# Optimization experiments

Hardware: AMD Instinct MI355X
Metric: run time of the kernel (lower is better)

The kernel has to match this reference:

```python
import jax, jax.numpy as jnp
import numpy as np

B, S, D_IN, D_OUT = 4, 2048, 2048, 2048
EPS = 1e-10


def setup_inputs() -> dict:
    key = jax.random.key(0)
    kx, kw, kb = jax.random.split(key, 3)
    x = jax.random.normal(kx, (B, S, D_IN), dtype=jnp.float32)
    weight = jax.random.normal(kw, (D_OUT, D_IN), dtype=jnp.float32) * 0.02
    bias = jax.random.normal(kb, (D_OUT,), dtype=jnp.float32) * 0.02
    return {"x": x, "weight": weight, "bias": bias}


def reference(x, weight, bias):
    # abs-mean scale over the whole weight matrix (scalar)
    scale = jnp.mean(jnp.abs(weight))
    # ternary quantization: round(w/scale) clamped to {-1, 0, 1}
    w_t = jnp.clip(jnp.round(weight / (scale + EPS)), -1.0, 1.0)
    # straight-through estimator: forward uses w_t*scale, grad flows to weight
    w_ste = weight + jax.lax.stop_gradient(w_t * scale - weight)
    # F.linear: x @ w_ste.T + bias
    return jnp.einsum('bsi,oi->bso', x, w_ste) + bias
```

## Files before the change

kernel.cpp:

```cpp
#include <hip/hip_runtime.h>
#include <hip/hip_bf16.h>
#include <stdint.h>

#define M_DIM 8192
#define N_DIM 2048
#define K_DIM 2048
#define NT    (K_DIM / 64)

typedef float f32x4 __attribute__((ext_vector_type(4)));
typedef short bf16x8 __attribute__((ext_vector_type(8)));

typedef const __attribute__((address_space(1))) char* gp_t;
typedef __attribute__((address_space(3))) char* lp_t;

static __device__ __forceinline__ void gload_lds16(const void* g, void* l) {
  __builtin_amdgcn_global_load_lds((gp_t)(uintptr_t)g, (lp_t)(uint32_t)(uintptr_t)l, 16, 0, 0);
}

static __device__ __forceinline__ unsigned short f2bf(float f) {
  unsigned int u = __float_as_uint(f);
  unsigned int r = (u + 0x7FFFu + ((u >> 16) & 1u)) >> 16;
  return (unsigned short)r;
}

__global__ void cvt_x_absum(const float* __restrict__ x, unsigned short* __restrict__ xb,
                            const float* __restrict__ w, float* __restrict__ partials) {
  const int b = blockIdx.x;
  if (b < 16384) {
    int tid = b * 256 + threadIdx.x;
    float4 v = ((const float4*)x)[tid];
    ushort4 o;
    o.x = f2bf(v.x); o.y = f2bf(v.y); o.z = f2bf(v.z); o.w = f2bf(v.w);
    ((ushort4*)xb)[tid] = o;
  } else {
    int tid = (b - 16384) * 256 + threadIdx.x;
    const float4* w4 = (const float4*)w;
    float s = 0.f;
#pragma unroll
    for (int i = 0; i < 4; ++i) {
      float4 v = w4[tid + i * 262144];
      s += fabsf(v.x) + fabsf(v.y) + fabsf(v.z) + fabsf(v.w);
    }
#pragma unroll
    for (int off = 32; off > 0; off >>= 1) s += __shfl_down(s, off, 64);
    __shared__ float ls[4];
    if ((threadIdx.x & 63) == 0) ls[threadIdx.x >> 6] = s;
    __syncthreads();
    if (threadIdx.x == 0) partials[b - 16384] = (ls[0] + ls[1]) + (ls[2] + ls[3]);
  }
}

__global__ void quant_w(const float* __restrict__ w, const float* __restrict__ partials,
                        unsigned short* __restrict__ wt, float* __restrict__ scale_out) {
  __shared__ float ls[4];
  float s = 0.f;
#pragma unroll
  for (int i = 0; i < 4; ++i) s += partials[threadIdx.x + i * 256];
#pragma unroll
  for (int off = 32; off > 0; off >>= 1) s += __shfl_down(s, off, 64);
  if ((threadIdx.x & 63) == 0) ls[threadIdx.x >> 6] = s;
  __syncthreads();
  const float scale = ((ls[0] + ls[1]) + (ls[2] + ls[3])) * (1.0f / 4194304.0f);
  if (blockIdx.x == 0 && threadIdx.x == 0) scale_out[0] = scale;

  const float inv = 1.0f / (scale + 1e-10f);
  int tid = blockIdx.x * 256 + threadIdx.x;
  float4 v = ((const float4*)w)[tid];
  ushort4 o;
  float t;
  t = fminf(1.f, fmaxf(-1.f, rintf(v.x * inv))); o.x = f2bf(t);
  t = fminf(1.f, fmaxf(-1.f, rintf(v.y * inv))); o.y = f2bf(t);
  t = fminf(1.f, fmaxf(-1.f, rintf(v.z * inv))); o.z = f2bf(t);
  t = fminf(1.f, fmaxf(-1.f, rintf(v.w * inv))); o.w = f2bf(t);
  ((ushort4*)wt)[tid] = o;
}


#define VMCNT(n) asm volatile("s_waitcnt vmcnt(" #n ")" ::: "memory")
#define FENCE    asm volatile("" ::: "memory")
#define BARRIER  do { FENCE; __builtin_amdgcn_s_barrier(); FENCE; } while (0)

#define READ_A(base, mh, dst)                                                                   \
  do {                                                                                          \
    _Pragma("unroll") for (int i = 0; i < 4; ++i) {                                             \
      dst[i][0] = *(const bf16x8*)((base) + (wr * 128 + (mh) * 64 + i * 16) * 128 + rd0);       \
      dst[i][1] = *(const bf16x8*)((base) + (wr * 128 + (mh) * 64 + i * 16) * 128 + rd1);       \
    }                                                                                           \
  } while (0)

#define READ_B(base, nh, dst)                                                                   \
  do {                                                                                          \
    _Pragma("unroll") for (int j = 0; j < 2; ++j) {                                             \
      dst[j][0] = *(const bf16x8*)((base) + (wc * 64 + (nh) * 32 + j * 16) * 128 + rd0);        \
      dst[j][1] = *(const bf16x8*)((base) + (wc * 64 + (nh) * 32 + j * 16) * 128 + rd1);        \
    }                                                                                           \
  } while (0)

#define MFMA_Q(mh, nh, ar, br)                                                                  \
  do {                                                                                          \
    __builtin_amdgcn_s_setprio(1);                                                              \
    _Pragma("unroll") for (int i = 0; i < 4; ++i)                                               \
      _Pragma("unroll") for (int j = 0; j < 2; ++j)                                             \
        acc[(mh) * 4 + i][(nh) * 2 + j] = __builtin_amdgcn_mfma_f32_16x16x32_bf16(              \
            ar[i][0], br[j][0], acc[(mh) * 4 + i][(nh) * 2 + j], 0, 0, 0);                      \
    _Pragma("unroll") for (int i = 0; i < 4; ++i)                                               \
      _Pragma("unroll") for (int j = 0; j < 2; ++j)                                             \
        acc[(mh) * 4 + i][(nh) * 2 + j] = __builtin_amdgcn_mfma_f32_16x16x32_bf16(              \
            ar[i][1], br[j][1], acc[(mh) * 4 + i][(nh) * 2 + j], 0, 0, 0);                      \
    __builtin_amdgcn_s_setprio(0);                                                              \
  } while (0)

#define SA(bufsel, r) gload_lds16(Ag + offA[r] + ktA, ldsb + (bufsel) * 65536 + tid * 16 + (r) * 8192)
#define SB(bufsel, r) gload_lds16(Bg + offB[r] + ktB, ldsb + (bufsel) * 65536 + 32768 + tid * 16 + (r) * 8192)

#define TILE_BODY(CURSEL, NXTSEL, t)                                                            \
  do {                                                                                          \
    const char* curA = ldsb + (CURSEL) * 65536;                                                 \
    const char* curB = curA + 32768;                                                            \
    READ_A(curA, 0, a0);                                                                        \
    READ_B(curB, 0, b0);                                                                        \
    if ((t) < NT - 1) { SA(NXTSEL, 0); SA(NXTSEL, 1); }                                         \
    MFMA_Q(0, 0, a0, b0);                                                                       \
    READ_B(curB, 1, b1);                                                                        \
    if ((t) < NT - 1) { SA(NXTSEL, 2); SA(NXTSEL, 3); ktA += 128; }                             \
    MFMA_Q(0, 1, a0, b1);                                                                       \
    BARRIER;        \
    READ_A(curA, 1, a1);                                                                        \
    if ((t) < NT - 2) { SB(CURSEL, 0); SB(CURSEL, 1); }                                         \
    MFMA_Q(1, 0, a1, b0);                                                                       \
    if ((t) < NT - 2) {                                                                         \
      SB(CURSEL, 2); SB(CURSEL, 3); ktB += 128;                                                 \
      VMCNT(4);                \
    } else {                                                                                    \
      VMCNT(0);                                                                                 \
    }                                                                                           \
    MFMA_Q(1, 1, a1, b1);                                                                       \
    BARRIER;                                  \
  } while (0)

__global__ void __launch_bounds__(512, 2)
gemm_bt(const unsigned short* __restrict__ A, const unsigned short* __restrict__ Bt,
        const float* __restrict__ bias, const float* __restrict__ scale_p,
        float* __restrict__ out) {
  __shared__ __align__(16) char lds_raw[131072];
  char* ldsb = (char*)lds_raw;

  const int tid = threadIdx.x;
  const int lane = tid & 63;
  const int wid = tid >> 6;
  const int wr = wid >> 2;
  const int wc = wid & 3;
  const int l15 = lane & 15, lhi = lane >> 4;

  const int swzl = (l15 & 7) << 4;
  const int rd0 = l15 * 128 + ((lhi * 16) ^ swzl);
  const int rd1 = l15 * 128 + (((lhi * 16) ^ 64) ^ swzl);

  const int bid = blockIdx.x;
  const int swz = (bid & 7) * 32 + (bid >> 3);
  const int bm = swz >> 3;
  const int bn = swz & 7;
  const int m0 = bm << 8, n0 = bn << 8;

  const int srow = tid >> 3;
  const int scol = (((tid & 7) ^ ((tid >> 3) & 7)) << 4);
  const char* Ag = (const char*)A;
  const char* Bg = (const char*)Bt;
  uint32_t offA[4], offB[4];
#pragma unroll
  for (int r = 0; r < 4; ++r) {
    offA[r] = (uint32_t)(m0 + srow + r * 64) * (K_DIM * 2) + scol;
    offB[r] = (uint32_t)(n0 + srow + r * 64) * (K_DIM * 2) + scol;
  }
  uint32_t ktA = 0, ktB = 0;

  f32x4 acc[8][4];
#pragma unroll
  for (int m = 0; m < 8; ++m)
#pragma unroll
    for (int n = 0; n < 4; ++n) {
      f32x4 z = {0.f, 0.f, 0.f, 0.f};
      acc[m][n] = z;
    }

  SA(0, 0); SA(0, 1); SA(0, 2); SA(0, 3);
  SB(0, 0); SB(0, 1); SB(0, 2); SB(0, 3);
  ktB = 128;
  SB(1, 0); SB(1, 1); SB(1, 2); SB(1, 3);
  ktA = 128; ktB = 256;
  VMCNT(4);
  BARRIER;

  bf16x8 a0[4][2], a1[4][2], b0[2][2], b1[2][2];

  for (int it = 0; it < NT / 2; ++it) {
    const int t0 = 2 * it;
    TILE_BODY(0, 1, t0);
    TILE_BODY(1, 0, t0 + 1);
  }

  const float scale = scale_p[0];
#pragma unroll
  for (int n = 0; n < 4; ++n) {
    const int col = n0 + wc * 64 + n * 16 + l15;
    const float bv = bias[col];
#pragma unroll
    for (int m = 0; m < 8; ++m) {
      const int r0 = m0 + wr * 128 + m * 16 + lhi * 4;
      float* op = out + (size_t)r0 * N_DIM + col;
#pragma unroll
      for (int j = 0; j < 4; ++j) op[(size_t)j * N_DIM] = acc[m][n][j] * scale + bv;
    }
  }
}

extern "C" void kernel_launch(void* const* d_in, const int* in_sizes, int n_in,
                              void* d_out, int out_size, void* d_ws, size_t ws_size,
                              hipStream_t stream) {
  (void)in_sizes; (void)n_in; (void)out_size; (void)ws_size;
  const float* x    = (const float*)d_in[0];
  const float* w    = (const float*)d_in[1];
  const float* bias = (const float*)d_in[2];
  float* out = (float*)d_out;

  float* partials = (float*)d_ws;
  float* scale_slot = partials + 1024;
  unsigned short* wt = (unsigned short*)((char*)d_ws + 8192);
  unsigned short* xb = (unsigned short*)((char*)d_ws + 8192 + (size_t)N_DIM * K_DIM * 2);

  cvt_x_absum<<<17408, 256, 0, stream>>>(x, xb, w, partials);
  quant_w<<<4096, 256, 0, stream>>>(w, partials, wt, scale_slot);
  gemm_bt<<<256, 512, 0, stream>>>(xb, wt, bias, scale_slot, out);
}
```

Baseline: 82.94 us.

## Switch GEMM inner loop from 16x16x32 to 32x32x16 bf16 MFMA tiles

Replaces the 16x16x32 MFMA instructions with 32x32x16 MFMA, restructuring LDS fragment reads, accumulator layout (f32x16 per 32x32 tile) and the epilogue store mapping. Larger MFMA tiles need fewer LDS fragment reads per FLOP and fewer instruction issues, which raises compute density. The swizzled LDS read pattern changes to 32-row lanes, so bank conflicts and the epilogue's strided stores may behave differently.

```diff
diff --git a/kernel.cpp b/kernel.cpp
--- a/kernel.cpp
+++ b/kernel.cpp
@@ -8,6 +8,7 @@
 #define NT    (K_DIM / 64)
 
 typedef float f32x4 __attribute__((ext_vector_type(4)));
+typedef float f32x16 __attribute__((ext_vector_type(16)));
 typedef short bf16x8 __attribute__((ext_vector_type(8)));
 
 typedef const __attribute__((address_space(1))) char* gp_t;
@@ -82,31 +83,28 @@
 
 #define READ_A(base, mh, dst)                                                                   \
   do {                                                                                          \
-    _Pragma("unroll") for (int i = 0; i < 4; ++i) {                                             \
-      dst[i][0] = *(const bf16x8*)((base) + (wr * 128 + (mh) * 64 + i * 16) * 128 + rd0);       \
-      dst[i][1] = *(const bf16x8*)((base) + (wr * 128 + (mh) * 64 + i * 16) * 128 + rd1);       \
-    }                                                                                           \
+    _Pragma("unroll") for (int mb2 = 0; mb2 < 2; ++mb2)                                         \
+      _Pragma("unroll") for (int ks = 0; ks < 4; ++ks)                                          \
+        dst[mb2][ks] = *(const bf16x8*)((base) +                                                \
+            (wr * 128 + ((mh) * 2 + mb2) * 32 + l31) * 128 +                                    \
+            ((ks * 32 + lh1 * 16) ^ swzB));                                                     \
   } while (0)
 
 #define READ_B(base, nh, dst)                                                                   \
   do {                                                                                          \
-    _Pragma("unroll") for (int j = 0; j < 2; ++j) {                                             \
-      dst[j][0] = *(const bf16x8*)((base) + (wc * 64 + (nh) * 32 + j * 16) * 128 + rd0);        \
-      dst[j][1] = *(const bf16x8*)((base) + (wc * 64 + (nh) * 32 + j * 16) * 128 + rd1);        \
-    }                                                                                           \
+    _Pragma("unroll") for (int ks = 0; ks < 4; ++ks)                                            \
+      dst[ks] = *(const bf16x8*)((base) +                                                       \
+          (wc * 64 + (nh) * 32 + l31) * 128 +                                                   \
+          ((ks * 32 + lh1 * 16) ^ swzB));                                                       \
   } while (0)
 
 #define MFMA_Q(mh, nh, ar, br)                                                                  \
   do {                                                                                          \
     __builtin_amdgcn_s_setprio(1);                                                              \
-    _Pragma("unroll") for (int i = 0; i < 4; ++i)                                               \
-      _Pragma("unroll") for (int j = 0; j < 2; ++j)                                             \
-        acc[(mh) * 4 + i][(nh) * 2 + j] = __builtin_amdgcn_mfma_f32_16x16x32_bf16(              \
-            ar[i][0], br[j][0], acc[(mh) * 4 + i][(nh) * 2 + j], 0, 0, 0);                      \
-    _Pragma("unroll") for (int i = 0; i < 4; ++i)                                               \
-      _Pragma("unroll") for (int j = 0; j < 2; ++j)                                             \
-        acc[(mh) * 4 + i][(nh) * 2 + j] = __builtin_amdgcn_mfma_f32_16x16x32_bf16(              \
-            ar[i][1], br[j][1], acc[(mh) * 4 + i][(nh) * 2 + j], 0, 0, 0);                      \
+    _Pragma("unroll") for (int ks = 0; ks < 4; ++ks)                                            \
+      _Pragma("unroll") for (int mb2 = 0; mb2 < 2; ++mb2)                                       \
+        acc[(mh) * 2 + mb2][nh] = __builtin_amdgcn_mfma_f32_32x32x16_bf16(                      \
+            ar[mb2][ks], br[ks], acc[(mh) * 2 + mb2][nh], 0, 0, 0);                             \
     __builtin_amdgcn_s_setprio(0);                                                              \
   } while (0)
 
@@ -150,11 +148,9 @@
   const int wid = tid >> 6;
   const int wr = wid >> 2;
   const int wc = wid & 3;
-  const int l15 = lane & 15, lhi = lane >> 4;
-
-  const int swzl = (l15 & 7) << 4;
-  const int rd0 = l15 * 128 + ((lhi * 16) ^ swzl);
-  const int rd1 = l15 * 128 + (((lhi * 16) ^ 64) ^ swzl);
+  const int l31 = lane & 31, lh1 = lane >> 5;
+
+  const int swzB = (l31 & 7) << 4;
 
   const int bid = blockIdx.x;
   const int swz = (bid & 7) * 32 + (bid >> 3);
@@ -174,14 +170,16 @@
   }
   uint32_t ktA = 0, ktB = 0;
 
-  f32x4 acc[8][4];
-#pragma unroll
-  for (int m = 0; m < 8; ++m)
-#pragma unroll
-    for (int n = 0; n < 4; ++n) {
-      f32x4 z = {0.f, 0.f, 0.f, 0.f};
-      acc[m][n] = z;
-    }
+  f32x16 acc[4][2];
+  {
+    f32x16 z;
+#pragma unroll
+    for (int e = 0; e < 16; ++e) z[e] = 0.f;
+#pragma unroll
+    for (int m = 0; m < 4; ++m)
+#pragma unroll
+      for (int n = 0; n < 2; ++n) acc[m][n] = z;
+  }
 
   SA(0, 0); SA(0, 1); SA(0, 2); SA(0, 3);
   SB(0, 0); SB(0, 1); SB(0, 2); SB(0, 3);
@@ -191,7 +189,7 @@
   VMCNT(4);
   BARRIER;
 
-  bf16x8 a0[4][2], a1[4][2], b0[2][2], b1[2][2];
+  bf16x8 a0[2][4], a1[2][4], b0[4], b1[4];
 
   for (int it = 0; it < NT / 2; ++it) {
     const int t0 = 2 * it;
@@ -201,15 +199,18 @@
 
   const float scale = scale_p[0];
 #pragma unroll
-  for (int n = 0; n < 4; ++n) {
-    const int col = n0 + wc * 64 + n * 16 + l15;
+  for (int nb = 0; nb < 2; ++nb) {
+    const int col = n0 + wc * 64 + nb * 32 + l31;
     const float bv = bias[col];
 #pragma unroll
-    for (int m = 0; m < 8; ++m) {
-      const int r0 = m0 + wr * 128 + m * 16 + lhi * 4;
-      float* op = out + (size_t)r0 * N_DIM + col;
-#pragma unroll
-      for (int j = 0; j < 4; ++j) op[(size_t)j * N_DIM] = acc[m][n][j] * scale + bv;
+    for (int mb = 0; mb < 4; ++mb) {
+      const int rbase = m0 + wr * 128 + mb * 32 + 4 * lh1;
+      float* op = out + (size_t)rbase * N_DIM + col;
+#pragma unroll
+      for (int reg = 0; reg < 16; ++reg) {
+        const int roff = (reg & 3) + 8 * (reg >> 2);
+        op[(size_t)roff * N_DIM] = acc[mb][nb][reg] * scale + bv;
+      }
     }
   }
 }
```

New measurement: 93.73 us. 13.0% more time.

## Pre-swizzle ternary weights into MFMA fragment layout and load B directly to registers

Applied to the files above, without the earlier changes.

The weight quantization kernel now writes the bf16 ternary weights in a layout already arranged per MFMA fragment, so each lane can fetch its B operand with one contiguous 16-byte global load. The GEMM drops the LDS staging of B and register-prefetches the next tile's B fragments, which halves LDS use and removes B LDS reads. In exchange each wave separately loads B from global/L2 with no sharing across the block. The pipeline is also simplified to a full vmcnt(0) wait and one barrier per tile, which may expose more latency.

```diff
diff --git a/kernel.cpp b/kernel.cpp
--- a/kernel.cpp
+++ b/kernel.cpp
@@ -64,15 +64,29 @@
   if (blockIdx.x == 0 && threadIdx.x == 0) scale_out[0] = scale;
 
   const float inv = 1.0f / (scale + 1e-10f);
-  int tid = blockIdx.x * 256 + threadIdx.x;
-  float4 v = ((const float4*)w)[tid];
-  ushort4 o;
+  const int i = blockIdx.x * 256 + threadIdx.x;
+  const int n = i >> 8;
+  const int j = i & 255;
+  float4 v0 = ((const float4*)w)[i * 2];
+  float4 v1 = ((const float4*)w)[i * 2 + 1];
+  bf16x8 o;
   float t;
-  t = fminf(1.f, fmaxf(-1.f, rintf(v.x * inv))); o.x = f2bf(t);
-  t = fminf(1.f, fmaxf(-1.f, rintf(v.y * inv))); o.y = f2bf(t);
-  t = fminf(1.f, fmaxf(-1.f, rintf(v.z * inv))); o.z = f2bf(t);
-  t = fminf(1.f, fmaxf(-1.f, rintf(v.w * inv))); o.w = f2bf(t);
-  ((ushort4*)wt)[tid] = o;
+  t = fminf(1.f, fmaxf(-1.f, rintf(v0.x * inv))); o[0] = (short)f2bf(t);
+  t = fminf(1.f, fmaxf(-1.f, rintf(v0.y * inv))); o[1] = (short)f2bf(t);
+  t = fminf(1.f, fmaxf(-1.f, rintf(v0.z * inv))); o[2] = (short)f2bf(t);
+  t = fminf(1.f, fmaxf(-1.f, rintf(v0.w * inv))); o[3] = (short)f2bf(t);
+  t = fminf(1.f, fmaxf(-1.f, rintf(v1.x * inv))); o[4] = (short)f2bf(t);
+  t = fminf(1.f, fmaxf(-1.f, rintf(v1.y * inv))); o[5] = (short)f2bf(t);
+  t = fminf(1.f, fmaxf(-1.f, rintf(v1.z * inv))); o[6] = (short)f2bf(t);
+  t = fminf(1.f, fmaxf(-1.f, rintf(v1.w * inv))); o[7] = (short)f2bf(t);
+
+  const int tt  = j >> 3;
+  const int kh  = (j >> 2) & 1;
+  const int lhi = j & 3;
+  const int n16 = n >> 4;
+  const int l15 = n & 15;
+  const uint32_t byte = ((((uint32_t)tt * 128 + n16) * 2 + kh) << 10) + (lhi * 16 + l15) * 16;
+  *(bf16x8*)((char*)wt + byte) = o;
 }
 
 
@@ -88,61 +102,52 @@
     }                                                                                           \
   } while (0)
 
-#define READ_B(base, nh, dst)                                                                   \
-  do {                                                                                          \
-    _Pragma("unroll") for (int j = 0; j < 2; ++j) {                                             \
-      dst[j][0] = *(const bf16x8*)((base) + (wc * 64 + (nh) * 32 + j * 16) * 128 + rd0);        \
-      dst[j][1] = *(const bf16x8*)((base) + (wc * 64 + (nh) * 32 + j * 16) * 128 + rd1);        \
-    }                                                                                           \
-  } while (0)
-
-#define MFMA_Q(mh, nh, ar, br)                                                                  \
+#define LOADB(dst, tt)                                                                          \
+  do {                                                                                          \
+    _Pragma("unroll") for (int nh = 0; nh < 2; ++nh)                                            \
+      _Pragma("unroll") for (int j = 0; j < 2; ++j)                                             \
+        _Pragma("unroll") for (int kh = 0; kh < 2; ++kh)                                        \
+          dst[nh][j][kh] = *(const bf16x8*)(Bp + (size_t)(tt) * 262144 + bOff[nh * 2 + j][kh]); \
+  } while (0)
+
+#define MFMA_Q(mh, nh, ar, bc)                                                                  \
   do {                                                                                          \
     __builtin_amdgcn_s_setprio(1);                                                              \
     _Pragma("unroll") for (int i = 0; i < 4; ++i)                                               \
       _Pragma("unroll") for (int j = 0; j < 2; ++j)                                             \
         acc[(mh) * 4 + i][(nh) * 2 + j] = __builtin_amdgcn_mfma_f32_16x16x32_bf16(              \
-            ar[i][0], br[j][0], acc[(mh) * 4 + i][(nh) * 2 + j], 0, 0, 0);                      \
+            ar[i][0], bc[nh][j][0], acc[(mh) * 4 + i][(nh) * 2 + j], 0, 0, 0);                  \
     _Pragma("unroll") for (int i = 0; i < 4; ++i)                                               \
       _Pragma("unroll") for (int j = 0; j < 2; ++j)                                             \
         acc[(mh) * 4 + i][(nh) * 2 + j] = __builtin_amdgcn_mfma_f32_16x16x32_bf16(              \
-            ar[i][1], br[j][1], acc[(mh) * 4 + i][(nh) * 2 + j], 0, 0, 0);                      \
+            ar[i][1], bc[nh][j][1], acc[(mh) * 4 + i][(nh) * 2 + j], 0, 0, 0);                  \
     __builtin_amdgcn_s_setprio(0);                                                              \
   } while (0)
 
-#define SA(bufsel, r) gload_lds16(Ag + offA[r] + ktA, ldsb + (bufsel) * 65536 + tid * 16 + (r) * 8192)
-#define SB(bufsel, r) gload_lds16(Bg + offB[r] + ktB, ldsb + (bufsel) * 65536 + 32768 + tid * 16 + (r) * 8192)
-
-#define TILE_BODY(CURSEL, NXTSEL, t)                                                            \
-  do {                                                                                          \
-    const char* curA = ldsb + (CURSEL) * 65536;                                                 \
-    const char* curB = curA + 32768;                                                            \
-    READ_A(curA, 0, a0);                                                                        \
-    READ_B(curB, 0, b0);                                                                        \
-    if ((t) < NT - 1) { SA(NXTSEL, 0); SA(NXTSEL, 1); }                                         \
-    MFMA_Q(0, 0, a0, b0);                                                                       \
-    READ_B(curB, 1, b1);                                                                        \
-    if ((t) < NT - 1) { SA(NXTSEL, 2); SA(NXTSEL, 3); ktA += 128; }                             \
-    MFMA_Q(0, 1, a0, b1);                                                                       \
-    BARRIER;        \
-    READ_A(curA, 1, a1);                                                                        \
-    if ((t) < NT - 2) { SB(CURSEL, 0); SB(CURSEL, 1); }                                         \
-    MFMA_Q(1, 0, a1, b0);                                                                       \
-    if ((t) < NT - 2) {                                                                         \
-      SB(CURSEL, 2); SB(CURSEL, 3); ktB += 128;                                                 \
-      VMCNT(4);                \
-    } else {                                                                                    \
-      VMCNT(0);                                                                                 \
+#define SA(bufsel, r) gload_lds16(Ag + offA[r] + ktA, ldsb + (bufsel) * 32768 + tid * 16 + (r) * 8192)
+
+#define TILE_BODY(CURSEL, NXTSEL, bc, bnx, t)                                                   \
+  do {                                                                                          \
+    const char* curA = ldsb + (CURSEL) * 32768;                                                 \
+    if ((t) < NT - 1) {                                                                         \
+      SA(NXTSEL, 0); SA(NXTSEL, 1); SA(NXTSEL, 2); SA(NXTSEL, 3); ktA += 128;                   \
+      LOADB(bnx, (t) + 1);                                                                      \
     }                                                                                           \
-    MFMA_Q(1, 1, a1, b1);                                                                       \
-    BARRIER;                                  \
+    READ_A(curA, 0, a);                                                                         \
+    MFMA_Q(0, 0, a, bc);                                                                        \
+    MFMA_Q(0, 1, a, bc);                                                                        \
+    READ_A(curA, 1, a);                                                                         \
+    MFMA_Q(1, 0, a, bc);                                                                        \
+    MFMA_Q(1, 1, a, bc);                                                                        \
+    VMCNT(0);                \
+    BARRIER;           \
   } while (0)
 
 __global__ void __launch_bounds__(512, 2)
 gemm_bt(const unsigned short* __restrict__ A, const unsigned short* __restrict__ Bt,
         const float* __restrict__ bias, const float* __restrict__ scale_p,
         float* __restrict__ out) {
-  __shared__ __align__(16) char lds_raw[131072];
+  __shared__ __align__(16) char lds_raw[65536];
   char* ldsb = (char*)lds_raw;
 
   const int tid = threadIdx.x;
@@ -165,14 +170,19 @@
   const int srow = tid >> 3;
   const int scol = (((tid & 7) ^ ((tid >> 3) & 7)) << 4);
   const char* Ag = (const char*)A;
-  const char* Bg = (const char*)Bt;
-  uint32_t offA[4], offB[4];
-#pragma unroll
-  for (int r = 0; r < 4; ++r) {
+  const char* Bp = (const char*)Bt;
+  uint32_t offA[4];
+#pragma unroll
+  for (int r = 0; r < 4; ++r)
     offA[r] = (uint32_t)(m0 + srow + r * 64) * (K_DIM * 2) + scol;
-    offB[r] = (uint32_t)(n0 + srow + r * 64) * (K_DIM * 2) + scol;
-  }
-  uint32_t ktA = 0, ktB = 0;
+  uint32_t ktA = 0;
+
+  uint32_t bOff[4][2];
+#pragma unroll
+  for (int fn = 0; fn < 4; ++fn)
+#pragma unroll
+    for (int kh = 0; kh < 2; ++kh)
+      bOff[fn][kh] = ((((uint32_t)(bn * 16 + wc * 4 + fn)) * 2 + kh) << 10) + lane * 16;
 
   f32x4 acc[8][4];
 #pragma unroll
@@ -183,20 +193,18 @@
       acc[m][n] = z;
     }
 
+  bf16x8 a[4][2], bA[2][2][2], bB[2][2][2];
+
   SA(0, 0); SA(0, 1); SA(0, 2); SA(0, 3);
-  SB(0, 0); SB(0, 1); SB(0, 2); SB(0, 3);
-  ktB = 128;
-  SB(1, 0); SB(1, 1); SB(1, 2); SB(1, 3);
-  ktA = 128; ktB = 256;
-  VMCNT(4);
+  LOADB(bA, 0);
+  ktA = 128;
+  VMCNT(0);
   BARRIER;
-
-  bf16x8 a0[4][2], a1[4][2], b0[2][2], b1[2][2];
 
   for (int it = 0; it < NT / 2; ++it) {
     const int t0 = 2 * it;
-    TILE_BODY(0, 1, t0);
-    TILE_BODY(1, 0, t0 + 1);
+    TILE_BODY(0, 1, bA, bB, t0);
+    TILE_BODY(1, 0, bB, bA, t0 + 1);
   }
 
   const float scale = scale_p[0];
@@ -229,6 +237,6 @@
   unsigned short* xb = (unsigned short*)((char*)d_ws + 8192 + (size_t)N_DIM * K_DIM * 2);
 
   cvt_x_absum<<<17408, 256, 0, stream>>>(x, xb, w, partials);
-  quant_w<<<4096, 256, 0, stream>>>(w, partials, wt, scale_slot);
+  quant_w<<<2048, 256, 0, stream>>>(w, partials, wt, scale_slot);
   gemm_bt<<<256, 512, 0, stream>>>(xb, wt, bias, scale_slot, out);
 }
```

Result: slower. 131.4 us (+58.4%).
